# Kernel optimization log

Hardware: AMD Instinct MI355X
Metric: run time of the kernel (lower is better)

Reference implementation:

```python
import jax, jax.numpy as jnp
import numpy as np

B, Q, Fn, E, NL, L = 32, 16, 4096, 256, 8, 2


def _mapper(x, W, b):
    # stack of residual blocks: relu(x @ W + b) + x (dropout=0 at eval)
    for i in range(W.shape[0]):
        x = jax.nn.relu(x @ W[i] + b[i]) + x
    return x


def setup_inputs() -> dict:
    key = jax.random.key(0)
    ks = jax.random.split(key, 10)
    s = 1.0 / np.sqrt(E)
    return {
        "query": jax.random.normal(ks[0], (B, Q, E), jnp.float32),
        "features": jax.random.normal(ks[1], (B, Fn, E), jnp.float32),
        "values": jax.random.normal(ks[2], (B, Fn, E), jnp.float32),
        "attention_mask": jnp.ones((B, Fn), jnp.float32),
        "feature_time_weights": jax.random.uniform(ks[3], (B, Fn), jnp.float32),
        "Wq": jax.random.normal(ks[4], (L, E, E), jnp.float32) * s,
        "bq": jnp.zeros((L, E), jnp.float32),
        "Wf": jax.random.normal(ks[5], (L, E, E), jnp.float32) * s,
        "bf": jnp.zeros((L, E), jnp.float32),
        "Wv": jax.random.normal(ks[6], (L, E, E), jnp.float32) * s,
        "bv": jnp.zeros((L, E), jnp.float32),
        "Wc": jax.random.normal(ks[7], (L, E, E), jnp.float32) * s,
        "bc": jnp.zeros((L, E), jnp.float32),
        "Wout": jax.random.normal(ks[8], (E, NL), jnp.float32) * s,
        "bout": jnp.zeros((NL,), jnp.float32),
    }


def reference(query, features, values, attention_mask, feature_time_weights,
              Wq, bq, Wf, bf, Wv, bv, Wc, bc, Wout, bout):
    q = _mapper(query, Wq, bq)           # [B,Q,E]
    f = _mapper(features, Wf, bf)        # [B,F,E]
    # broadcast dot-product gate, done as batched matmul instead of repeat()
    attn = jax.nn.sigmoid(jnp.einsum('bqd,bfd->bqf', q, f))  # [B,Q,F]
    v = _mapper(values, Wv, bv)          # [B,F,E]
    w = attn * feature_time_weights[:, None, :] * attention_mask[:, None, :]
    pooled = jnp.einsum('bfe,bqf->bqe', v, w)  # weighted value pooling
    h = _mapper(pooled, Wc, bc)
    return h @ Wout + bout               # [B,Q,num_labels]
```

## Files before the change

### kernel.cpp

```cpp
#include <hip/hip_runtime.h>
#include <hip/hip_bf16.h>

#define B_   32
#define Q_   16
#define F_   4096
#define E_   256
#define NL_  8
#define FT   64
#define NTB  16
#define CH   4
#define TPB  512

typedef __attribute__((ext_vector_type(8))) __bf16 bf16x8_t;
typedef __attribute__((ext_vector_type(4))) __bf16 bf16x4_t;
typedef __attribute__((ext_vector_type(4))) float  f32x4;

__device__ __forceinline__ int swz(int r) {
  return ((r & 7) << 4) ^ (((r >> 3) & 3) << 5);
}
__device__ __forceinline__ int xoff(int r, int c2) {
  return r * 512 + (c2 ^ swz(r));
}
__device__ __forceinline__ unsigned short f2bf_bits(float f) {
  __bf16 h = (__bf16)f;
  return __builtin_bit_cast(unsigned short, h);
}

__global__ __launch_bounds__(256) void prep_kernel(
    const float* __restrict__ Wf, const float* __restrict__ Wv,
    const float* __restrict__ Wq, const float* __restrict__ Wc,
    unsigned short* __restrict__ WtF, unsigned short* __restrict__ WtV,
    unsigned short* __restrict__ WqT, unsigned short* __restrict__ WcT) {
  const int blk = blockIdx.x;
  const int t = threadIdx.x;
  __shared__ float ts[64][65];
  const int mat = blk >> 4;
  const int t16 = blk & 15;
  const int k0 = (t16 >> 2) * 64, n0 = (t16 & 3) * 64;
  const float* src;
  if (mat < 2) src = Wf + mat * 65536;
  else if (mat < 4) src = Wv + (mat - 2) * 65536;
  else if (mat < 6) src = Wq + (mat - 4) * 65536;
  else src = Wc + (mat - 6) * 65536;
#pragma unroll
  for (int p = 0; p < 16; ++p) {
    int e = p * 256 + t;
    int kk = e >> 6, nn = e & 63;
    ts[nn][kk] = src[(k0 + kk) * 256 + n0 + nn];
  }
  __syncthreads();
  unsigned short* dst;
  if (mat < 2) dst = WtF + mat * 65536;
  else if (mat < 4) dst = WtV + (mat - 2) * 65536;
  else if (mat < 6) dst = WqT + (mat - 4) * 65536;
  else dst = WcT + (mat - 6) * 65536;
#pragma unroll
  for (int p = 0; p < 16; ++p) {
    int e = p * 256 + t;
    int nn = e >> 6, kk = e & 63;
    dst[(n0 + nn) * 256 + k0 + kk] = f2bf_bits(ts[nn][kk]);
  }
}

__device__ __forceinline__ void stage_tile(char* Xs, const float* __restrict__ src, int tid) {
  f32x4 v[8];
#pragma unroll
  for (int j = 0; j < 4; ++j) {
    int u = j * 512 + tid;
    int r = u >> 5;
    int c8 = (u & 31) << 3;
    const f32x4* p = (const f32x4*)(src + (size_t)r * E_ + c8);
    v[2 * j]     = __builtin_nontemporal_load(p);
    v[2 * j + 1] = __builtin_nontemporal_load(p + 1);
  }
#pragma unroll
  for (int j = 0; j < 4; ++j) {
    int u = j * 512 + tid;
    int r = u >> 5;
    int cb = (u & 31) << 4;
    f32x4 a = v[2 * j], b = v[2 * j + 1];
    bf16x8_t o;
    o[0] = (__bf16)a[0]; o[1] = (__bf16)a[1]; o[2] = (__bf16)a[2]; o[3] = (__bf16)a[3];
    o[4] = (__bf16)b[0]; o[5] = (__bf16)b[1]; o[6] = (__bf16)b[2]; o[7] = (__bf16)b[3];
    *(bf16x8_t*)(Xs + xoff(r, cb)) = o;
  }
}

__device__ __forceinline__ void layer_ip(char* __restrict__ X,
                                         const unsigned short* __restrict__ Wt,
                                         const float* __restrict__ bias, int w, int lane) {
  const int c16 = lane & 15, g = lane >> 4, kb = g << 3;
  const unsigned short* r0 = Wt + (w * 32 + c16) * E_ + kb;
  const unsigned short* r1 = Wt + (w * 32 + 16 + c16) * E_ + kb;

  bf16x8_t wa0[8], wa1[8];
#pragma unroll
  for (int ks = 0; ks < 8; ++ks) {
    wa0[ks] = *(const bf16x8_t*)(r0 + ks * 32);
    wa1[ks] = *(const bf16x8_t*)(r1 + ks * 32);
  }
  __builtin_amdgcn_sched_barrier(0);

  f32x4 acc[2][4];
#pragma unroll
  for (int ef = 0; ef < 2; ++ef)
#pragma unroll
    for (int mf = 0; mf < 4; ++mf) acc[ef][mf] = (f32x4){0.f, 0.f, 0.f, 0.f};

#pragma unroll
  for (int ks = 0; ks < 8; ++ks) {
    const int k = ks * 32 + kb;
#pragma unroll
    for (int mf = 0; mf < 4; ++mf) {
      bf16x8_t xb = *(const bf16x8_t*)(X + xoff(mf * 16 + c16, k << 1));
      acc[0][mf] = __builtin_amdgcn_mfma_f32_16x16x32_bf16(wa0[ks], xb, acc[0][mf], 0, 0, 0);
      acc[1][mf] = __builtin_amdgcn_mfma_f32_16x16x32_bf16(wa1[ks], xb, acc[1][mf], 0, 0, 0);
    }
  }
  __syncthreads();
#pragma unroll
  for (int ef = 0; ef < 2; ++ef) {
    const int e0 = w * 32 + ef * 16 + (g << 2);
    const float4 b4 = *(const float4*)(bias + e0);
#pragma unroll
    for (int mf = 0; mf < 4; ++mf) {
      const int m = mf * 16 + c16;
      bf16x4_t* p = (bf16x4_t*)(X + xoff(m, e0 << 1));
      bf16x4_t old = *p;
      bf16x4_t nw;
      nw[0] = (__bf16)(fmaxf(acc[ef][mf][0] + b4.x, 0.f) + (float)old[0]);
      nw[1] = (__bf16)(fmaxf(acc[ef][mf][1] + b4.y, 0.f) + (float)old[1]);
      nw[2] = (__bf16)(fmaxf(acc[ef][mf][2] + b4.z, 0.f) + (float)old[2]);
      nw[3] = (__bf16)(fmaxf(acc[ef][mf][3] + b4.w, 0.f) + (float)old[3]);
      *p = nw;
    }
  }
  __syncthreads();
}

__global__ __launch_bounds__(TPB) void qmap_kernel(
    const float* __restrict__ query, const unsigned short* __restrict__ WqT,
    const float* __restrict__ bq, unsigned short* __restrict__ qmb) {
  const int blk = blockIdx.x;
  const int tid = threadIdx.x;
  const int lane = tid & 63, w = tid >> 6;

  __shared__ __align__(128) char X[32768];

  stage_tile(X, query + (size_t)blk * 64 * E_, tid);
  __syncthreads();

  layer_ip(X, WqT, bq, w, lane);
  layer_ip(X, WqT + 65536, bq + E_, w, lane);

#pragma unroll
  for (int j = 0; j < 4; ++j) {
    int u = j * 512 + tid;
    int r = u >> 5;
    bf16x8_t v = *(const bf16x8_t*)(X + xoff(r, (u & 31) << 4));
    *(bf16x8_t*)(qmb + (size_t)(blk * 64 + r) * E_ + ((u & 31) << 3)) = v;
  }
}

__global__ __launch_bounds__(TPB) void passA_kernel(
    const float* __restrict__ features,
    const float* __restrict__ amask, const float* __restrict__ ftw,
    const unsigned short* __restrict__ WtF, const float* __restrict__ bfb,
    const unsigned short* __restrict__ qmb, unsigned short* __restrict__ Wsg) {
  const int bid0 = blockIdx.x;
  const int bid = (bid0 & 7) * 64 + (bid0 >> 3);
  const int b = bid >> 4, tb = bid & 15;
  const int tid = threadIdx.x;
  const int lane = tid & 63, w = tid >> 6;
  const int c16 = lane & 15, g = lane >> 4, kb = g << 3;

  __shared__ __align__(128) char X[2][32768];

  const float* srcB = features + (size_t)(b * F_ + tb * CH * FT) * E_;

  stage_tile(X[0], srcB, tid);
  __syncthreads();
  int cur = 0;

  for (int c = 0; c < CH; ++c) {
    if (c + 1 < CH) stage_tile(X[cur ^ 1], srcB + (size_t)(c + 1) * FT * E_, tid);

    layer_ip(X[cur], WtF, bfb, w, lane);
    layer_ip(X[cur], WtF + 65536, bfb + E_, w, lane);

    if (w < 4) {
      const int f0 = (tb * CH + c) * FT;
      f32x4 sv = (f32x4){0.f, 0.f, 0.f, 0.f};
      const int fl = w * 16 + c16;
      const unsigned short* qbase = qmb + (size_t)(b * Q_ + c16) * E_ + kb;
#pragma unroll
      for (int ks = 0; ks < 8; ++ks) {
        bf16x8_t qa = *(const bf16x8_t*)(qbase + ks * 32);
        bf16x8_t xb = *(const bf16x8_t*)(X[cur] + xoff(fl, (ks * 32 + kb) << 1));
        sv = __builtin_amdgcn_mfma_f32_16x16x32_bf16(qa, xb, sv, 0, 0, 0);
      }
      const int fg = f0 + fl;
      const float lw = ftw[b * F_ + fg] * amask[b * F_ + fg];
#pragma unroll
      for (int r = 0; r < 4; ++r) {
        float sg = 1.f / (1.f + __expf(-sv[r]));
        Wsg[((size_t)(b * Q_ + g * 4 + r)) * F_ + fg] = f2bf_bits(sg * lw);
      }
    }
    __syncthreads();
    cur ^= 1;
  }
}

__global__ __launch_bounds__(TPB) void passB_kernel(
    const float* __restrict__ values,
    const unsigned short* __restrict__ WtV, const float* __restrict__ bvb,
    const unsigned short* __restrict__ Wsg, float* __restrict__ partials) {
  const int bid0 = blockIdx.x;
  const int bid = (bid0 & 7) * 64 + (bid0 >> 3);
  const int b = bid >> 4, tb = bid & 15;
  const int tid = threadIdx.x;
  const int lane = tid & 63, w = tid >> 6;
  const int c16 = lane & 15, g = lane >> 4, kb = g << 3;

  __shared__ __align__(128) char X[2][32768];
  __shared__ __align__(16) unsigned short Wl[Q_][FT + 8];

  const float* srcB = values + (size_t)(b * F_ + tb * CH * FT) * E_;

  f32x4 pacc[2];
  pacc[0] = (f32x4){0.f, 0.f, 0.f, 0.f};
  pacc[1] = (f32x4){0.f, 0.f, 0.f, 0.f};

  stage_tile(X[0], srcB, tid);
  __syncthreads();
  int cur = 0;

  for (int c = 0; c < CH; ++c) {
    const int f0 = (tb * CH + c) * FT;
    if (c + 1 < CH) stage_tile(X[cur ^ 1], srcB + (size_t)(c + 1) * FT * E_, tid);

    layer_ip(X[cur], WtV, bvb, w, lane);

#pragma unroll
    for (int kk = 0; kk < 2; ++kk) {
      int idx = tid + kk * 512;
      int q = idx >> 6, j = idx & 63;
      Wl[q][j] = Wsg[((size_t)(b * Q_ + q)) * F_ + f0 + j];
    }

    layer_ip(X[cur], WtV + 65536, bvb + E_, w, lane);

#pragma unroll
    for (int ks = 0; ks < FT / 32; ++ks) {
      bf16x8_t a = *(const bf16x8_t*)&Wl[c16][ks * 32 + kb];
#pragma unroll
      for (int nf = 0; nf < 2; ++nf) {
        const int e = w * 32 + nf * 16 + c16;
        bf16x8_t bb;
#pragma unroll
        for (int i = 0; i < 8; ++i) {
          const int f = ks * 32 + kb + i;
          bb[i] = *(const __bf16*)(X[cur] + xoff(f, e << 1));
        }
        pacc[nf] = __builtin_amdgcn_mfma_f32_16x16x32_bf16(a, bb, pacc[nf], 0, 0, 0);
      }
    }
    __syncthreads();
    cur ^= 1;
  }

#pragma unroll
  for (int nf = 0; nf < 2; ++nf) {
    const int e = w * 32 + nf * 16 + c16;
#pragma unroll
    for (int r = 0; r < 4; ++r) {
      const int q = g * 4 + r;
      partials[(((size_t)b * NTB + tb) * Q_ + q) * E_ + e] = pacc[nf][r];
    }
  }
}

__global__ __launch_bounds__(TPB) void tail_kernel(
    const float* __restrict__ partials, const unsigned short* __restrict__ WcT,
    const float* __restrict__ bc, const float* __restrict__ Wout,
    const float* __restrict__ bout, float* __restrict__ out) {
  const int blk = blockIdx.x;
  const int tid = threadIdx.x;
  const int lane = tid & 63, w = tid >> 6;

  __shared__ __align__(128) char X[32768];

#pragma unroll
  for (int j = 0; j < 4; ++j) {
    int u = j * 512 + tid;
    int rl = u >> 5;
    int R = blk * 64 + rl;
    int b = R >> 4, q = R & 15;
    int e0 = (u & 31) << 3;
    f32x4 s0 = (f32x4){0.f, 0.f, 0.f, 0.f};
    f32x4 s1 = (f32x4){0.f, 0.f, 0.f, 0.f};
#pragma unroll
    for (int tb = 0; tb < NTB; ++tb) {
      const f32x4* p = (const f32x4*)(partials + (((size_t)(b * NTB + tb)) * Q_ + q) * E_ + e0);
      s0 += p[0];
      s1 += p[1];
    }
    bf16x8_t o;
    o[0] = (__bf16)s0[0]; o[1] = (__bf16)s0[1]; o[2] = (__bf16)s0[2]; o[3] = (__bf16)s0[3];
    o[4] = (__bf16)s1[0]; o[5] = (__bf16)s1[1]; o[6] = (__bf16)s1[2]; o[7] = (__bf16)s1[3];
    *(bf16x8_t*)(X + xoff(rl, e0 << 1)) = o;
  }
  __syncthreads();

  layer_ip(X, WcT, bc, w, lane);
  layer_ip(X, WcT + 65536, bc + E_, w, lane);

  {
    const int rl = tid >> 3, n = tid & 7;
    const int R = blk * 64 + rl;
    float sum = bout[n];
#pragma unroll
    for (int k0 = 0; k0 < E_; k0 += 8) {
      bf16x8_t h8 = *(const bf16x8_t*)(X + xoff(rl, k0 << 1));
#pragma unroll
      for (int i = 0; i < 8; ++i)
        sum += (float)h8[i] * Wout[(k0 + i) * NL_ + n];
    }
    out[R * NL_ + n] = sum;
  }
}

extern "C" void kernel_launch(void* const* d_in, const int* in_sizes, int n_in,
                              void* d_out, int out_size, void* d_ws, size_t ws_size,
                              hipStream_t stream) {
  (void)in_sizes; (void)n_in; (void)out_size; (void)ws_size;
  const float* query    = (const float*)d_in[0];
  const float* features = (const float*)d_in[1];
  const float* values   = (const float*)d_in[2];
  const float* amask    = (const float*)d_in[3];
  const float* ftw      = (const float*)d_in[4];
  const float* Wq       = (const float*)d_in[5];
  const float* bq       = (const float*)d_in[6];
  const float* Wf       = (const float*)d_in[7];
  const float* bfb      = (const float*)d_in[8];
  const float* Wv       = (const float*)d_in[9];
  const float* bvb      = (const float*)d_in[10];
  const float* Wc       = (const float*)d_in[11];
  const float* bcb      = (const float*)d_in[12];
  const float* Wout     = (const float*)d_in[13];
  const float* bout     = (const float*)d_in[14];
  float* out = (float*)d_out;

  char* ws = (char*)d_ws;
  unsigned short* WtF = (unsigned short*)(ws);
  unsigned short* WtV = (unsigned short*)(ws + 262144);
  unsigned short* WqT = (unsigned short*)(ws + 524288);
  unsigned short* WcT = (unsigned short*)(ws + 786432);
  unsigned short* qmb = (unsigned short*)(ws + 1048576);
  unsigned short* Wsg = (unsigned short*)(ws + 1310720);
  float* partials     = (float*)(ws + 5505024);

  prep_kernel<<<128, 256, 0, stream>>>(Wf, Wv, Wq, Wc, WtF, WtV, WqT, WcT);
  qmap_kernel<<<(B_ * Q_) / 64, TPB, 0, stream>>>(query, WqT, bq, qmb);
  passA_kernel<<<B_ * NTB, TPB, 0, stream>>>(features, amask, ftw,
                                             WtF, bfb, qmb, Wsg);
  passB_kernel<<<B_ * NTB, TPB, 0, stream>>>(values, WtV, bvb, Wsg, partials);
  tail_kernel<<<(B_ * Q_) / 64, TPB, 0, stream>>>(partials, WcT, bcb, Wout, bout, out);
}
```

Baseline: 232.0 us.

## Drop LDS double buffering and shrink register footprint to raise occupancy

PassA and passB now use a single 32 KB LDS tile instead of two, staging each chunk synchronously before compute, and declare launch bounds with a minimum of 6 blocks. Weight fragments in layer_ip are prefetched one k-step ahead instead of all 8 being held in registers, and stage_tile converts each load pair straight away instead of buffering 8 vectors. The goal is to cut LDS and VGPR use so more blocks fit per CU and overlap comes from occupancy, not intra-block prefetch. The cost is that loads and compute inside a block are no longer overlapped, and a barrier is added per chunk.

```diff
diff --git a/kernel.cpp b/kernel.cpp
--- a/kernel.cpp
+++ b/kernel.cpp
@@ -63,26 +63,18 @@
 }
 
 __device__ __forceinline__ void stage_tile(char* Xs, const float* __restrict__ src, int tid) {
-  f32x4 v[8];
 #pragma unroll
   for (int j = 0; j < 4; ++j) {
     int u = j * 512 + tid;
     int r = u >> 5;
     int c8 = (u & 31) << 3;
     const f32x4* p = (const f32x4*)(src + (size_t)r * E_ + c8);
-    v[2 * j]     = __builtin_nontemporal_load(p);
-    v[2 * j + 1] = __builtin_nontemporal_load(p + 1);
-  }
-#pragma unroll
-  for (int j = 0; j < 4; ++j) {
-    int u = j * 512 + tid;
-    int r = u >> 5;
-    int cb = (u & 31) << 4;
-    f32x4 a = v[2 * j], b = v[2 * j + 1];
+    f32x4 a = __builtin_nontemporal_load(p);
+    f32x4 b = __builtin_nontemporal_load(p + 1);
     bf16x8_t o;
     o[0] = (__bf16)a[0]; o[1] = (__bf16)a[1]; o[2] = (__bf16)a[2]; o[3] = (__bf16)a[3];
     o[4] = (__bf16)b[0]; o[5] = (__bf16)b[1]; o[6] = (__bf16)b[2]; o[7] = (__bf16)b[3];
-    *(bf16x8_t*)(Xs + xoff(r, cb)) = o;
+    *(bf16x8_t*)(Xs + xoff(r, (u & 31) << 4)) = o;
   }
 }
 
@@ -93,29 +85,29 @@
   const unsigned short* r0 = Wt + (w * 32 + c16) * E_ + kb;
   const unsigned short* r1 = Wt + (w * 32 + 16 + c16) * E_ + kb;
 
-  bf16x8_t wa0[8], wa1[8];
+  f32x4 acc[2][4];
+#pragma unroll
+  for (int ef = 0; ef < 2; ++ef)
+#pragma unroll
+    for (int mf = 0; mf < 4; ++mf) acc[ef][mf] = (f32x4){0.f, 0.f, 0.f, 0.f};
+
+  bf16x8_t wa0 = *(const bf16x8_t*)(r0);
+  bf16x8_t wa1 = *(const bf16x8_t*)(r1);
 #pragma unroll
   for (int ks = 0; ks < 8; ++ks) {
-    wa0[ks] = *(const bf16x8_t*)(r0 + ks * 32);
-    wa1[ks] = *(const bf16x8_t*)(r1 + ks * 32);
-  }
-  __builtin_amdgcn_sched_barrier(0);
-
-  f32x4 acc[2][4];
-#pragma unroll
-  for (int ef = 0; ef < 2; ++ef)
-#pragma unroll
-    for (int mf = 0; mf < 4; ++mf) acc[ef][mf] = (f32x4){0.f, 0.f, 0.f, 0.f};
-
-#pragma unroll
-  for (int ks = 0; ks < 8; ++ks) {
+    bf16x8_t nx0 = wa0, nx1 = wa1;
+    if (ks < 7) {
+      nx0 = *(const bf16x8_t*)(r0 + (ks + 1) * 32);
+      nx1 = *(const bf16x8_t*)(r1 + (ks + 1) * 32);
+    }
     const int k = ks * 32 + kb;
 #pragma unroll
     for (int mf = 0; mf < 4; ++mf) {
       bf16x8_t xb = *(const bf16x8_t*)(X + xoff(mf * 16 + c16, k << 1));
-      acc[0][mf] = __builtin_amdgcn_mfma_f32_16x16x32_bf16(wa0[ks], xb, acc[0][mf], 0, 0, 0);
-      acc[1][mf] = __builtin_amdgcn_mfma_f32_16x16x32_bf16(wa1[ks], xb, acc[1][mf], 0, 0, 0);
-    }
+      acc[0][mf] = __builtin_amdgcn_mfma_f32_16x16x32_bf16(wa0, xb, acc[0][mf], 0, 0, 0);
+      acc[1][mf] = __builtin_amdgcn_mfma_f32_16x16x32_bf16(wa1, xb, acc[1][mf], 0, 0, 0);
+    }
+    wa0 = nx0; wa1 = nx1;
   }
   __syncthreads();
 #pragma unroll
@@ -162,7 +154,7 @@
   }
 }
 
-__global__ __launch_bounds__(TPB) void passA_kernel(
+__global__ __launch_bounds__(TPB, 6) void passA_kernel(
     const float* __restrict__ features,
     const float* __restrict__ amask, const float* __restrict__ ftw,
     const unsigned short* __restrict__ WtF, const float* __restrict__ bfb,
@@ -174,19 +166,16 @@
   const int lane = tid & 63, w = tid >> 6;
   const int c16 = lane & 15, g = lane >> 4, kb = g << 3;
 
-  __shared__ __align__(128) char X[2][32768];
+  __shared__ __align__(128) char X[32768];
 
   const float* srcB = features + (size_t)(b * F_ + tb * CH * FT) * E_;
 
-  stage_tile(X[0], srcB, tid);
-  __syncthreads();
-  int cur = 0;
-
   for (int c = 0; c < CH; ++c) {
-    if (c + 1 < CH) stage_tile(X[cur ^ 1], srcB + (size_t)(c + 1) * FT * E_, tid);
-
-    layer_ip(X[cur], WtF, bfb, w, lane);
-    layer_ip(X[cur], WtF + 65536, bfb + E_, w, lane);
+    stage_tile(X, srcB + (size_t)c * FT * E_, tid);
+    __syncthreads();
+
+    layer_ip(X, WtF, bfb, w, lane);
+    layer_ip(X, WtF + 65536, bfb + E_, w, lane);
 
     if (w < 4) {
       const int f0 = (tb * CH + c) * FT;
@@ -196,7 +185,7 @@
 #pragma unroll
       for (int ks = 0; ks < 8; ++ks) {
         bf16x8_t qa = *(const bf16x8_t*)(qbase + ks * 32);
-        bf16x8_t xb = *(const bf16x8_t*)(X[cur] + xoff(fl, (ks * 32 + kb) << 1));
+        bf16x8_t xb = *(const bf16x8_t*)(X + xoff(fl, (ks * 32 + kb) << 1));
         sv = __builtin_amdgcn_mfma_f32_16x16x32_bf16(qa, xb, sv, 0, 0, 0);
       }
       const int fg = f0 + fl;
@@ -208,11 +197,10 @@
       }
     }
     __syncthreads();
-    cur ^= 1;
-  }
-}
-
-__global__ __launch_bounds__(TPB) void passB_kernel(
+  }
+}
+
+__global__ __launch_bounds__(TPB, 6) void passB_kernel(
     const float* __restrict__ values,
     const unsigned short* __restrict__ WtV, const float* __restrict__ bvb,
     const unsigned short* __restrict__ Wsg, float* __restrict__ partials) {
@@ -223,7 +211,7 @@
   const int lane = tid & 63, w = tid >> 6;
   const int c16 = lane & 15, g = lane >> 4, kb = g << 3;
 
-  __shared__ __align__(128) char X[2][32768];
+  __shared__ __align__(128) char X[32768];
   __shared__ __align__(16) unsigned short Wl[Q_][FT + 8];
 
   const float* srcB = values + (size_t)(b * F_ + tb * CH * FT) * E_;
@@ -232,15 +220,12 @@
   pacc[0] = (f32x4){0.f, 0.f, 0.f, 0.f};
   pacc[1] = (f32x4){0.f, 0.f, 0.f, 0.f};
 
-  stage_tile(X[0], srcB, tid);
-  __syncthreads();
-  int cur = 0;
-
   for (int c = 0; c < CH; ++c) {
     const int f0 = (tb * CH + c) * FT;
-    if (c + 1 < CH) stage_tile(X[cur ^ 1], srcB + (size_t)(c + 1) * FT * E_, tid);
-
-    layer_ip(X[cur], WtV, bvb, w, lane);
+    stage_tile(X, srcB + (size_t)c * FT * E_, tid);
+    __syncthreads();
+
+    layer_ip(X, WtV, bvb, w, lane);
 
 #pragma unroll
     for (int kk = 0; kk < 2; ++kk) {
@@ -249,7 +234,7 @@
       Wl[q][j] = Wsg[((size_t)(b * Q_ + q)) * F_ + f0 + j];
     }
 
-    layer_ip(X[cur], WtV + 65536, bvb + E_, w, lane);
+    layer_ip(X, WtV + 65536, bvb + E_, w, lane);
 
 #pragma unroll
     for (int ks = 0; ks < FT / 32; ++ks) {
@@ -261,13 +246,12 @@
 #pragma unroll
         for (int i = 0; i < 8; ++i) {
           const int f = ks * 32 + kb + i;
-          bb[i] = *(const __bf16*)(X[cur] + xoff(f, e << 1));
+          bb[i] = *(const __bf16*)(X + xoff(f, e << 1));
         }
         pacc[nf] = __builtin_amdgcn_mfma_f32_16x16x32_bf16(a, bb, pacc[nf], 0, 0, 0);
       }
     }
     __syncthreads();
-    cur ^= 1;
   }
 
 #pragma unroll
```

After: 443.8 us. +91.3%, slower.
